# Performance work log

Hardware: AMD Instinct MI355X
Metric: run time of the kernel (lower is better)

Reference implementation:

```python
import jax, jax.numpy as jnp
import numpy as np

DIM = 7
HID = 128
BATCH = 131072
CHOL = DIM * (DIM + 1) // 2  # 28
_TRIL_R, _TRIL_C = np.tril_indices(DIM)
_DIAG = np.arange(DIM)


def _mlp(x, W1, b1, W2, b2, W3, b3):
    h = jnp.tanh(x @ W1 + b1)
    h = jnp.tanh(h @ W2 + b2)
    return h @ W3 + b3


def _build_cholesky(raw):
    # raw: [..., CHOL] -> lower-triangular L [..., DIM, DIM], softplus diagonal for positivity
    L = jnp.zeros(raw.shape[:-1] + (DIM, DIM), raw.dtype)
    L = L.at[..., _TRIL_R, _TRIL_C].set(raw)
    L = L.at[..., _DIAG, _DIAG].set(jax.nn.softplus(L[..., _DIAG, _DIAG]))
    return L


def _spd(raw):
    L = _build_cholesky(raw)
    return L @ jnp.swapaxes(L, -1, -2)  # L L^T, SPD


def setup_inputs() -> dict:
    key = jax.random.key(0)
    ks = jax.random.split(key, 20)
    s = 0.1
    f = jnp.float32
    return {
        "q": jax.random.normal(ks[0], (BATCH, DIM), f),
        "dq": jax.random.normal(ks[1], (BATCH, DIM), f),
        "ddq": jax.random.normal(ks[2], (BATCH, DIM), f),
        "mW1": jax.random.normal(ks[3], (DIM, HID), f) * s,
        "mb1": jax.random.normal(ks[4], (HID,), f) * s,
        "mW2": jax.random.normal(ks[5], (HID, HID), f) * s,
        "mb2": jax.random.normal(ks[6], (HID,), f) * s,
        "mW3": jax.random.normal(ks[7], (HID, CHOL), f) * s,
        "mb3": jax.random.normal(ks[8], (CHOL,), f) * s,
        "dW1": jax.random.normal(ks[9], (2 * DIM, HID), f) * s,
        "db1": jax.random.normal(ks[10], (HID,), f) * s,
        "dW2": jax.random.normal(ks[11], (HID, HID), f) * s,
        "db2": jax.random.normal(ks[12], (HID,), f) * s,
        "dW3": jax.random.normal(ks[13], (HID, CHOL), f) * s,
        "db3": jax.random.normal(ks[14], (CHOL,), f) * s,
        "pW1": jax.random.normal(ks[15], (DIM, HID), f) * s,
        "pb1": jax.random.normal(ks[16], (HID,), f) * s,
        "pw2": jax.random.normal(ks[17], (HID,), f) * s,
    }


def reference(q, dq, ddq, mW1, mb1, mW2, mb2, mW3, mb3,
              dW1, db1, dW2, db2, dW3, db3, pW1, pb1, pw2):
    def M_single(qi):  # qi: [DIM] -> [DIM, DIM]
        return _spd(_mlp(qi, mW1, mb1, mW2, mb2, mW3, mb3))

    # Mass matrix M(q): [B, DIM, DIM]
    Mb = _spd(_mlp(q, mW1, mb1, mW2, mb2, mW3, mb3))

    # Full batched Jacobian dM[i,k]/dq[j] -> J[b,i,k,j], replaces DIM^3 autograd.grad loop
    J = jax.vmap(jax.jacfwd(M_single))(q)  # [B, DIM, DIM, DIM]

    # Coriolis: C[b,i,j] = 0.5 * sum_k (dM_ik/dq_j + dM_ij/dq_k - dM_jk/dq_i) * dq_k
    C = 0.5 * (jnp.einsum('bikj,bk->bij', J, dq)
               + jnp.einsum('bijk,bk->bij', J, dq)
               - jnp.einsum('bjki,bk->bij', J, dq))

    # Damping D(q, dq): [B, DIM, DIM]
    Db = _spd(_mlp(jnp.concatenate([q, dq], axis=1), dW1, db1, dW2, db2, dW3, db3))

    # Convex potential (1-hidden-layer ICNN) and its gradient
    def V_single(qi):
        h = jax.nn.softplus(qi @ pW1 + pb1)
        return h @ jax.nn.softplus(pw2)

    gradV = jax.vmap(jax.grad(V_single))(q)  # [B, DIM]

    tau = (jnp.einsum('bij,bj->bi', Mb, ddq)
           + jnp.einsum('bij,bj->bi', C + Db, dq)
           + gradV)
    return tau
```

## Files before the change

### kernel.cpp

```cpp
#include <hip/hip_runtime.h>

#define DIM 7
#define HID 128
#define CHOL 28

#define GRID_A 512
#define ITER_A 16
#define GRID_B 2048
#define ITER_B 4

#define PHASE_FENCE() __builtin_amdgcn_sched_barrier(0x7F)

typedef float    f32x4  __attribute__((ext_vector_type(4)));
typedef short    bf16x8 __attribute__((ext_vector_type(8)));
typedef unsigned uint4v __attribute__((ext_vector_type(4)));

__device__ __forceinline__ float tanh_f(float x){ float e=__expf(2.f*x); return 1.f - 2.f/(e+1.f); }
__device__ __forceinline__ float sig_f(float x){ return 1.f/(1.f+__expf(-x)); }
__device__ __forceinline__ float sp_f(float x){ return fmaxf(x,0.f) + __logf(1.f+__expf(-fabsf(x))); }

__device__ __forceinline__ unsigned short f2b(float v){
  unsigned u = __float_as_uint(v);
  u += 0x7FFFu + ((u>>16)&1u);
  return (unsigned short)(u>>16);
}
__device__ __forceinline__ bf16x8 as_bf(uint4v u){ union { uint4v a; bf16x8 f; } x; x.a=u; return x.f; }

__global__ void setup_frags(const float* __restrict__ mW2, const float* __restrict__ mW3,
                            const float* __restrict__ dW2, const float* __restrict__ dW3,
                            unsigned* __restrict__ ws){
  int idx = blockIdx.x*256 + threadIdx.x;
  if (idx < 8192) {
    int i2 = idx&3, f = idx>>2, l = f&63, st = f>>6;
    int s = st>>3, t = st&7;
    int k = 32*s + 8*(l>>4) + 2*i2, col = 16*t + (l&15);
    unsigned short lo = f2b(mW2[k*HID+col]), hi = f2b(mW2[(k+1)*HID+col]);
    ws[idx] = (unsigned)lo | ((unsigned)hi<<16);
  } else if (idx < 10240) {
    int j = idx-8192; int i2=j&3, f=j>>2, l=f&63, st=f>>6;
    int s = st>>1, t = st&1;
    int k = 32*s + 8*(l>>4) + 2*i2, col = 16*t + (l&15);
    float v0 = (col<CHOL) ? mW3[k*CHOL+col] : 0.f;
    float v1 = (col<CHOL) ? mW3[(k+1)*CHOL+col] : 0.f;
    ws[idx] = (unsigned)f2b(v0) | ((unsigned)f2b(v1)<<16);
  } else if (idx < 18432) {
    int j = idx-10240; int i2=j&3, f=j>>2, l=f&63, st=f>>6;
    int s = st>>3, t = st&7;
    int k = 32*s + 8*(l>>4) + 2*i2, col = 16*t + (l&15);
    unsigned short lo = f2b(dW2[k*HID+col]), hi = f2b(dW2[(k+1)*HID+col]);
    ws[idx] = (unsigned)lo | ((unsigned)hi<<16);
  } else if (idx < 20480) {
    int j = idx-18432; int i2=j&3, f=j>>2, l=f&63, st=f>>6;
    int s = st>>1, t = st&1;
    int k = 32*s + 8*(l>>4) + 2*i2, col = 16*t + (l&15);
    float v0 = (col<CHOL) ? dW3[k*CHOL+col] : 0.f;
    float v1 = (col<CHOL) ? dW3[(k+1)*CHOL+col] : 0.f;
    ws[idx] = (unsigned)f2b(v0) | ((unsigned)f2b(v1)<<16);
  }
}

__global__ __launch_bounds__(256, 2) void kernA(
    const float* __restrict__ q, const float* __restrict__ dq, const float* __restrict__ ddq,
    const float* __restrict__ mW1, const float* __restrict__ mb1,
    const float* __restrict__ mb2, const float* __restrict__ mb3,
    const float* __restrict__ pW1, const float* __restrict__ pb1, const float* __restrict__ pw2,
    const unsigned* __restrict__ ws, float* __restrict__ out)
{
  __shared__ __align__(16) unsigned short Abuf[4][2][16][HID];
  __shared__ __align__(16) uint4v W3lds[512];
  __shared__ float sbf[4][4][HID+8];
  __shared__ float pW1s[DIM][HID+8];
  __shared__ float rawb[4][4][8][CHOL];
  __shared__ float b2s[HID];
  __shared__ float b3s[CHOL];
  __shared__ float Lbs[4][4][CHOL], dLss[4][4][CHOL], dfs[4][4][CHOL];
  __shared__ float gvp2[4][4][14];
  __shared__ float wbs[4][4][DIM], ubs[4][4][DIM], vss[4][4][DIM];

  const int tid  = threadIdx.x;
  const int wid  = tid>>6;
  const int lane = tid&63;
  const int g4 = lane>>4, c = lane&15;
  const int R = lane&15, r7 = lane&7;

  if (tid < HID) b2s[tid] = mb2[tid];
  if (tid >= HID && tid < HID+CHOL) b3s[tid-HID] = mb3[tid-HID];
  for (int idx = tid; idx < DIM*HID; idx += 256) pW1s[idx>>7][idx&127] = pW1[idx];
  for (int idx = tid; idx < 512; idx += 256) W3lds[idx] = ((const uint4v*)(ws + 8192))[idx];

  float w1v0[DIM], w1v1[DIM], pw1v0[DIM], pw1v1[DIM];
#pragma unroll
  for (int j=0;j<DIM;++j){
    w1v0[j]=mW1[j*HID+lane];  w1v1[j]=mW1[j*HID+lane+64];
    pw1v0[j]=pW1[j*HID+lane]; pw1v1[j]=pW1[j*HID+lane+64];
  }
  const float b1v0=mb1[lane], b1v1=mb1[lane+64];
  const float pbv0=pb1[lane], pbv1=pb1[lane+64];
  const float sp0=sp_f(pw2[lane]), sp1=sp_f(pw2[lane+64]);

  const uint4v* __restrict__ W2f = (const uint4v*)ws;
  uint4v W2r[32];
#pragma unroll
  for (int i=0;i<32;++i) W2r[i] = W2f[i*64 + lane];

  __syncthreads();

  for (int it=0; it<ITER_A; ++it){
    const int ebase = (it*GRID_A + (int)blockIdx.x)*16 + wid*4;

    const int kb0 = lane>>3, ko = lane&7;
#pragma unroll
    for (int e=0;e<4;++e){
      const float* qp = q + (long)(ebase+e)*DIM;
      float qv[DIM];
#pragma unroll
      for (int j=0;j<DIM;++j) qv[j]=qp[j];
      const int mt = e>>1, R0 = 8*(e&1);
      {
        float z1=b1v0, zp=pbv0;
#pragma unroll
        for (int j=0;j<DIM;++j){ z1=fmaf(qv[j],w1v0[j],z1); zp=fmaf(qv[j],pw1v0[j],zp); }
        float h1=tanh_f(z1), g1=1.f-h1*h1;
        Abuf[wid][mt][R0][8*kb0 + ko] = f2b(h1);
#pragma unroll
        for (int j=0;j<DIM;++j)
          Abuf[wid][mt][R0+1+j][8*(kb0^(1+j)) + ko] = f2b(g1*w1v0[j]);
        sbf[wid][e][lane] = sig_f(zp)*sp0;
      }
      {
        float z1=b1v1, zp=pbv1;
#pragma unroll
        for (int j=0;j<DIM;++j){ z1=fmaf(qv[j],w1v1[j],z1); zp=fmaf(qv[j],pw1v1[j],zp); }
        float h1=tanh_f(z1), g1=1.f-h1*h1;
        const int kb1 = kb0+8;
        Abuf[wid][mt][R0][8*kb1 + ko] = f2b(h1);
#pragma unroll
        for (int j=0;j<DIM;++j)
          Abuf[wid][mt][R0+1+j][8*(kb1^(1+j)) + ko] = f2b(g1*w1v1[j]);
        sbf[wid][e][lane+64] = sig_f(zp)*sp1;
      }
    }
    PHASE_FENCE();

    bf16x8 Af0[4], Af1[4];
#pragma unroll
    for (int s=0;s<4;++s){
      const int blk = 8*((4*s+g4)^r7);
      Af0[s] = *(const bf16x8*)&Abuf[wid][0][R][blk];
      Af1[s] = *(const bf16x8*)&Abuf[wid][1][R][blk];
    }
    PHASE_FENCE();

#pragma unroll
    for (int t=0;t<8;++t){
      f32x4 a0 = f32x4{0.f,0.f,0.f,0.f};
      f32x4 a1 = f32x4{0.f,0.f,0.f,0.f};
#pragma unroll
      for (int s=0;s<4;++s){
        bf16x8 B = as_bf(W2r[s*8+t]);
        a0 = __builtin_amdgcn_mfma_f32_16x16x32_bf16(Af0[s],B,a0,0,0,0);
        a1 = __builtin_amdgcn_mfma_f32_16x16x32_bf16(Af1[s],B,a1,0,0,0);
      }
      const int col = 16*t+c;
      const int cb = col>>3, co = col&7;
      {
        const float z2  = a0[0] + b2s[col];
        const float h2o = tanh_f(z2);
        const float h2x = __shfl_xor(h2o, 16);
        const float h2  = (g4&1) ? h2x : h2o;
        const float g2  = 1.f - h2*h2;
#pragma unroll
        for (int reg=0;reg<4;++reg){
          const int Rr = 4*g4+reg;
          const int key = Rr&7;
          float v = g2*a0[reg];
          if (key==0) v = h2;
          Abuf[wid][0][Rr][8*(cb^key) + co] = f2b(v);
        }
      }
      {
        const float z2  = a1[0] + b2s[col];
        const float h2o = tanh_f(z2);
        const float h2x = __shfl_xor(h2o, 16);
        const float h2  = (g4&1) ? h2x : h2o;
        const float g2  = 1.f - h2*h2;
#pragma unroll
        for (int reg=0;reg<4;++reg){
          const int Rr = 4*g4+reg;
          const int key = Rr&7;
          float v = g2*a1[reg];
          if (key==0) v = h2;
          Abuf[wid][1][Rr][8*(cb^key) + co] = f2b(v);
        }
      }
    }
    PHASE_FENCE();

    f32x4 acc3[2][2];
#pragma unroll
    for (int a=0;a<2;++a){ acc3[a][0]=f32x4{0.f,0.f,0.f,0.f}; acc3[a][1]=f32x4{0.f,0.f,0.f,0.f}; }
#pragma unroll
    for (int s=0;s<4;++s){
      const int blk = 8*((4*s+g4)^r7);
      bf16x8 A0 = *(const bf16x8*)&Abuf[wid][0][R][blk];
      bf16x8 A1 = *(const bf16x8*)&Abuf[wid][1][R][blk];
#pragma unroll
      for (int nt=0;nt<2;++nt){
        bf16x8 B = as_bf(W3lds[(s*2+nt)*64 + lane]);
        acc3[0][nt] = __builtin_amdgcn_mfma_f32_16x16x32_bf16(A0,B,acc3[0][nt],0,0,0);
        acc3[1][nt] = __builtin_amdgcn_mfma_f32_16x16x32_bf16(A1,B,acc3[1][nt],0,0,0);
      }
    }

    if (c < 14){
      const int iv = (c<7)? c : c-7;
      const int nb = (c<7)? 0 : 64;
      float gp = 0.f;
#pragma unroll 8
      for (int nn=0; nn<64; ++nn)
        gp = fmaf(pW1s[iv][nb+nn], sbf[wid][g4][nb+nn], gp);
      gvp2[wid][g4][c] = gp;
    }

#pragma unroll
    for (int mt=0;mt<2;++mt){
      const int em = 2*mt + (g4>>1);
      const int rb = (g4&1)*4;
#pragma unroll
      for (int nt=0;nt<2;++nt){
        const int t = 16*nt+c;
        if (t < CHOL){
#pragma unroll
          for (int reg=0;reg<4;++reg) rawb[wid][em][rb+reg][t] = acc3[mt][nt][reg];
        }
      }
    }
    PHASE_FENCE();

    float dqv[DIM];
    {
      const float* dqp = dq + (long)(ebase+g4)*DIM;
#pragma unroll
      for (int j=0;j<DIM;++j) dqv[j]=dqp[j];
    }
#pragma unroll
    for (int h=0;h<2;++h){
      const int t = c + 16*h;
      if (t < CHOL){
        const float e0 = rawb[wid][g4][0][t] + b3s[t];
        const bool dg = (t==0)|(t==2)|(t==5)|(t==9)|(t==14)|(t==20)|(t==27);
        const float Lv = dg ? sp_f(e0) : e0;
        const float df = dg ? sig_f(e0) : 1.f;
        float s_=0.f;
#pragma unroll
        for (int j=0;j<DIM;++j) s_=fmaf(dqv[j], rawb[wid][g4][1+j][t], s_);
        Lbs[wid][g4][t]=Lv; dfs[wid][g4][t]=df; dLss[wid][g4][t]=df*s_;
      }
    }
    PHASE_FENCE();
    if (c < DIM){
      const float* ddqp = ddq + (long)(ebase+g4)*DIM;
      float wv=0.f, uv=0.f, vv=0.f;
#pragma unroll
      for (int r=0;r<DIM;++r){
        if (r>=c){
          const int id=r*(r+1)/2+c;
          const float Lrc = Lbs[wid][g4][id];
          wv=fmaf(Lrc,dqv[r],wv);
          uv=fmaf(Lrc,ddqp[r],uv);
          vv=fmaf(dLss[wid][g4][id],dqv[r],vv);
        }
      }
      wbs[wid][g4][c]=wv; ubs[wid][g4][c]=uv; vss[wid][g4][c]=vv;
    }
    PHASE_FENCE();
    if (c < DIM){
      const int i=c;
      float t12=0.f;
#pragma unroll
      for (int c2=0;c2<DIM;++c2){
        if (c2<=i){
          const int id=i*(i+1)/2+c2;
          t12=fmaf(Lbs[wid][g4][id], ubs[wid][g4][c2]+vss[wid][g4][c2], t12);
          t12=fmaf(dLss[wid][g4][id], wbs[wid][g4][c2], t12);
        }
      }
      const int TRt[CHOL]={0,1,1,2,2,2,3,3,3,3,4,4,4,4,4,5,5,5,5,5,5,6,6,6,6,6,6,6};
      const int TCt[CHOL]={0,0,1,0,1,2,0,1,2,3,0,1,2,3,4,0,1,2,3,4,5,0,1,2,3,4,5,6};
      float t3=0.f;
#pragma unroll
      for (int t=0;t<CHOL;++t)
        t3=fmaf(rawb[wid][g4][1+i][t]*dfs[wid][g4][t], dqv[TRt[t]]*wbs[wid][g4][TCt[t]], t3);
      out[(long)(ebase+g4)*DIM + i] = t12 - t3 + gvp2[wid][g4][i] + gvp2[wid][g4][7+i];
    }
    PHASE_FENCE();
  }
}

__global__ __launch_bounds__(64, 1) void kernB(
    const float* __restrict__ q, const float* __restrict__ dq,
    const float* __restrict__ dW1, const float* __restrict__ db1,
    const float* __restrict__ db2, const float* __restrict__ db3,
    const unsigned* __restrict__ ws, float* __restrict__ out)
{
  __shared__ __align__(16) unsigned short AbufD[16][HID];
  __shared__ float dW1s[2*DIM][HID];
  __shared__ float xsf[112+8], dsf[112+8];
  __shared__ float rawD[16][CHOL];
  __shared__ float LbD[16][CHOL];
  __shared__ float wdb[16][8];
  __shared__ float b2sD[HID];
  __shared__ float b3sD[CHOL];

  const int lane = threadIdx.x;
  const int g4 = lane>>4, c = lane&15;
  const int R = lane&15, rkey = lane&7;
  const int eL = lane>>2, sub = lane&3;

  b2sD[lane] = db2[lane]; b2sD[lane+64] = db2[lane+64];
  if (lane < CHOL) b3sD[lane] = db3[lane];
  for (int idx = lane; idx < 2*DIM*HID; idx += 64) dW1s[idx>>7][idx&127] = dW1[idx];
  const float b1v0 = db1[lane], b1v1 = db1[lane+64];

  const uint4v* __restrict__ W2fD = (const uint4v*)(ws + 10240);
  const uint4v* __restrict__ W3fD = (const uint4v*)(ws + 18432);
  uint4v W2rD[32];
#pragma unroll
  for (int i=0;i<32;++i) W2rD[i] = W2fD[i*64 + lane];
  uint4v W3rD[8];
#pragma unroll
  for (int i=0;i<8;++i)  W3rD[i] = W3fD[i*64 + lane];

  __syncthreads();

  for (int it=0; it<ITER_B; ++it){
    const int ebase = (it*GRID_B + (int)blockIdx.x)*16;

    for (int idx=lane; idx<112; idx+=64){
      xsf[idx] = q[(long)ebase*DIM + idx];
      dsf[idx] = dq[(long)ebase*DIM + idx];
    }
    PHASE_FENCE();

#pragma unroll
    for (int h=0; h<2; ++h){
      const int k = lane + 64*h;
      float z[16];
#pragma unroll
      for (int e=0;e<16;++e) z[e] = h ? b1v1 : b1v0;
#pragma unroll
      for (int j=0;j<DIM;++j){
        const float dj = dW1s[j][k & 127];
#pragma unroll
        for (int e=0;e<16;++e) z[e] = fmaf(xsf[7*e+j], dj, z[e]);
      }
#pragma unroll
      for (int j=0;j<DIM;++j){
        const float dj = dW1s[DIM+j][k & 127];
#pragma unroll
        for (int e=0;e<16;++e) z[e] = fmaf(dsf[7*e+j], dj, z[e]);
      }
      const int kb = k>>3, ko = k&7;
#pragma unroll
      for (int e=0;e<16;++e){
        AbufD[e][8*(kb^(e&7)) + ko] = f2b(tanh_f(z[e]));
      }
    }
    PHASE_FENCE();

    f32x4 acc[8];
#pragma unroll
    for (int b=0;b<8;++b) acc[b] = f32x4{0.f,0.f,0.f,0.f};
#pragma unroll
    for (int s=0;s<4;++s){
      const int blk = 8*((4*s+g4)^rkey);
      bf16x8 A0 = *(const bf16x8*)&AbufD[R][blk];
#pragma unroll
      for (int t=0;t<8;++t)
        acc[t] = __builtin_amdgcn_mfma_f32_16x16x32_bf16(A0, as_bf(W2rD[s*8+t]), acc[t], 0,0,0);
    }
    PHASE_FENCE();

#pragma unroll
    for (int t=0;t<8;++t){
      const int col = 16*t+c;
      const int cb = col>>3, co = col&7;
#pragma unroll
      for (int reg=0;reg<4;++reg){
        const int e = 4*g4+reg;
        const float h2 = tanh_f(acc[t][reg] + b2sD[col]);
        AbufD[e][8*(cb^(e&7)) + co] = f2b(h2);
      }
    }
    PHASE_FENCE();

    f32x4 acc3[2];
    acc3[0]=f32x4{0.f,0.f,0.f,0.f}; acc3[1]=f32x4{0.f,0.f,0.f,0.f};
#pragma unroll
    for (int s=0;s<4;++s){
      const int blk = 8*((4*s+g4)^rkey);
      bf16x8 A0 = *(const bf16x8*)&AbufD[R][blk];
#pragma unroll
      for (int nt=0;nt<2;++nt)
        acc3[nt] = __builtin_amdgcn_mfma_f32_16x16x32_bf16(A0, as_bf(W3rD[s*2+nt]), acc3[nt], 0,0,0);
    }

#pragma unroll
    for (int nt=0;nt<2;++nt){
      const int t = 16*nt+c;
      if (t < CHOL){
#pragma unroll
        for (int reg=0;reg<4;++reg) rawD[4*g4+reg][t] = acc3[nt][reg];
      }
    }
    PHASE_FENCE();

#pragma unroll
    for (int m=0;m<7;++m){
      const int t = 7*sub + m;
      const float e0 = rawD[eL][t] + b3sD[t];
      const bool dg = (t==0)|(t==2)|(t==5)|(t==9)|(t==14)|(t==20)|(t==27);
      LbD[eL][t] = dg ? sp_f(e0) : e0;
    }
    PHASE_FENCE();

    for (int cc = sub; cc < DIM; cc += 4){
      float wv = 0.f;
      for (int r = cc; r < DIM; ++r)
        wv = fmaf(LbD[eL][r*(r+1)/2 + cc], dsf[7*eL + r], wv);
      wdb[eL][cc] = wv;
    }
    PHASE_FENCE();

    for (int i0 = sub; i0 < DIM; i0 += 4){
      float td = 0.f;
      for (int cc = 0; cc <= i0; ++cc)
        td = fmaf(LbD[eL][i0*(i0+1)/2 + cc], wdb[eL][cc], td);
      out[(long)(ebase+eL)*DIM + i0] += td;
    }
    PHASE_FENCE();
  }
}

extern "C" void kernel_launch(void* const* d_in, const int* in_sizes, int n_in,
                              void* d_out, int out_size, void* d_ws, size_t ws_size,
                              hipStream_t stream) {
  const float* q   = (const float*)d_in[0];
  const float* dq  = (const float*)d_in[1];
  const float* ddq = (const float*)d_in[2];
  const float* mW1 = (const float*)d_in[3];
  const float* mb1 = (const float*)d_in[4];
  const float* mW2 = (const float*)d_in[5];
  const float* mb2 = (const float*)d_in[6];
  const float* mW3 = (const float*)d_in[7];
  const float* mb3 = (const float*)d_in[8];
  const float* dW1 = (const float*)d_in[9];
  const float* db1 = (const float*)d_in[10];
  const float* dW2 = (const float*)d_in[11];
  const float* db2 = (const float*)d_in[12];
  const float* dW3 = (const float*)d_in[13];
  const float* db3 = (const float*)d_in[14];
  const float* pW1 = (const float*)d_in[15];
  const float* pb1 = (const float*)d_in[16];
  const float* pw2 = (const float*)d_in[17];
  float* out = (float*)d_out;
  unsigned* wsu = (unsigned*)d_ws;

  hipLaunchKernelGGL(setup_frags, dim3(80), dim3(256), 0, stream, mW2, mW3, dW2, dW3, wsu);
  hipLaunchKernelGGL(kernA, dim3(GRID_A), dim3(256), 0, stream,
                     q, dq, ddq, mW1, mb1, mb2, mb3, pW1, pb1, pw2, (const unsigned*)wsu, out);
  hipLaunchKernelGGL(kernB, dim3(GRID_B), dim3(64), 0, stream,
                     q, dq, dW1, db1, db2, db3, (const unsigned*)wsu, out);
}
```

Baseline: 262.1 us.

## Move W2/W3 weight fragments from registers to LDS and widen blocks to 8 waves

New measurement: 233.8 us. -10.8%, faster.

```diff
diff --git a/kernel.cpp b/kernel.cpp
--- a/kernel.cpp
+++ b/kernel.cpp
@@ -4,9 +4,9 @@
 #define HID 128
 #define CHOL 28
 
-#define GRID_A 512
+#define GRID_A 256
 #define ITER_A 16
-#define GRID_B 2048
+#define GRID_B 256
 #define ITER_B 4
 
 #define PHASE_FENCE() __builtin_amdgcn_sched_barrier(0x7F)
@@ -23,6 +23,9 @@
   unsigned u = __float_as_uint(v);
   u += 0x7FFFu + ((u>>16)&1u);
   return (unsigned short)(u>>16);
+}
+__device__ __forceinline__ float b2f(unsigned short v){
+  return __uint_as_float(((unsigned)v)<<16);
 }
 __device__ __forceinline__ bf16x8 as_bf(uint4v u){ union { uint4v a; bf16x8 f; } x; x.a=u; return x.f; }
 
@@ -59,23 +62,24 @@
   }
 }
 
-__global__ __launch_bounds__(256, 2) void kernA(
+__global__ __launch_bounds__(512, 2) void kernA(
     const float* __restrict__ q, const float* __restrict__ dq, const float* __restrict__ ddq,
     const float* __restrict__ mW1, const float* __restrict__ mb1,
     const float* __restrict__ mb2, const float* __restrict__ mb3,
     const float* __restrict__ pW1, const float* __restrict__ pb1, const float* __restrict__ pw2,
     const unsigned* __restrict__ ws, float* __restrict__ out)
 {
-  __shared__ __align__(16) unsigned short Abuf[4][2][16][HID];
+  __shared__ __align__(16) unsigned short Abuf[8][2][16][HID];
+  __shared__ __align__(16) uint4v W2lds[2048];
   __shared__ __align__(16) uint4v W3lds[512];
-  __shared__ float sbf[4][4][HID+8];
+  __shared__ unsigned short sbf[8][4][HID];
+  __shared__ unsigned short rawb[8][4][8][CHOL];
   __shared__ float pW1s[DIM][HID+8];
-  __shared__ float rawb[4][4][8][CHOL];
   __shared__ float b2s[HID];
   __shared__ float b3s[CHOL];
-  __shared__ float Lbs[4][4][CHOL], dLss[4][4][CHOL], dfs[4][4][CHOL];
-  __shared__ float gvp2[4][4][14];
-  __shared__ float wbs[4][4][DIM], ubs[4][4][DIM], vss[4][4][DIM];
+  __shared__ float Lbs[8][4][CHOL], dLss[8][4][CHOL], dfs[8][4][CHOL];
+  __shared__ float gvp2[8][4][14];
+  __shared__ float wbs[8][4][DIM], ubs[8][4][DIM], vss[8][4][DIM];
 
   const int tid  = threadIdx.x;
   const int wid  = tid>>6;
@@ -85,8 +89,9 @@
 
   if (tid < HID) b2s[tid] = mb2[tid];
   if (tid >= HID && tid < HID+CHOL) b3s[tid-HID] = mb3[tid-HID];
-  for (int idx = tid; idx < DIM*HID; idx += 256) pW1s[idx>>7][idx&127] = pW1[idx];
-  for (int idx = tid; idx < 512; idx += 256) W3lds[idx] = ((const uint4v*)(ws + 8192))[idx];
+  for (int idx = tid; idx < DIM*HID; idx += 512) pW1s[idx>>7][idx&127] = pW1[idx];
+  for (int idx = tid; idx < 2048; idx += 512) W2lds[idx] = ((const uint4v*)ws)[idx];
+  for (int idx = tid; idx < 512;  idx += 512) W3lds[idx] = ((const uint4v*)(ws + 8192))[idx];
 
   float w1v0[DIM], w1v1[DIM], pw1v0[DIM], pw1v1[DIM];
 #pragma unroll
@@ -98,15 +103,10 @@
   const float pbv0=pb1[lane], pbv1=pb1[lane+64];
   const float sp0=sp_f(pw2[lane]), sp1=sp_f(pw2[lane+64]);
 
-  const uint4v* __restrict__ W2f = (const uint4v*)ws;
-  uint4v W2r[32];
-#pragma unroll
-  for (int i=0;i<32;++i) W2r[i] = W2f[i*64 + lane];
-
   __syncthreads();
 
   for (int it=0; it<ITER_A; ++it){
-    const int ebase = (it*GRID_A + (int)blockIdx.x)*16 + wid*4;
+    const int ebase = (it*GRID_A + (int)blockIdx.x)*32 + wid*4;
 
     const int kb0 = lane>>3, ko = lane&7;
 #pragma unroll
@@ -125,7 +125,7 @@
 #pragma unroll
         for (int j=0;j<DIM;++j)
           Abuf[wid][mt][R0+1+j][8*(kb0^(1+j)) + ko] = f2b(g1*w1v0[j]);
-        sbf[wid][e][lane] = sig_f(zp)*sp0;
+        sbf[wid][e][lane] = f2b(sig_f(zp)*sp0);
       }
       {
         float z1=b1v1, zp=pbv1;
@@ -137,7 +137,7 @@
 #pragma unroll
         for (int j=0;j<DIM;++j)
           Abuf[wid][mt][R0+1+j][8*(kb1^(1+j)) + ko] = f2b(g1*w1v1[j]);
-        sbf[wid][e][lane+64] = sig_f(zp)*sp1;
+        sbf[wid][e][lane+64] = f2b(sig_f(zp)*sp1);
       }
     }
     PHASE_FENCE();
@@ -157,7 +157,7 @@
       f32x4 a1 = f32x4{0.f,0.f,0.f,0.f};
 #pragma unroll
       for (int s=0;s<4;++s){
-        bf16x8 B = as_bf(W2r[s*8+t]);
+        bf16x8 B = as_bf(W2lds[(s*8+t)*64 + lane]);
         a0 = __builtin_amdgcn_mfma_f32_16x16x32_bf16(Af0[s],B,a0,0,0,0);
         a1 = __builtin_amdgcn_mfma_f32_16x16x32_bf16(Af1[s],B,a1,0,0,0);
       }
@@ -218,7 +218,7 @@
       float gp = 0.f;
 #pragma unroll 8
       for (int nn=0; nn<64; ++nn)
-        gp = fmaf(pW1s[iv][nb+nn], sbf[wid][g4][nb+nn], gp);
+        gp = fmaf(pW1s[iv][nb+nn], b2f(sbf[wid][g4][nb+nn]), gp);
       gvp2[wid][g4][c] = gp;
     }
 
@@ -231,7 +231,7 @@
         const int t = 16*nt+c;
         if (t < CHOL){
 #pragma unroll
-          for (int reg=0;reg<4;++reg) rawb[wid][em][rb+reg][t] = acc3[mt][nt][reg];
+          for (int reg=0;reg<4;++reg) rawb[wid][em][rb+reg][t] = f2b(acc3[mt][nt][reg]);
         }
       }
     }
@@ -247,13 +247,13 @@
     for (int h=0;h<2;++h){
       const int t = c + 16*h;
       if (t < CHOL){
-        const float e0 = rawb[wid][g4][0][t] + b3s[t];
+        const float e0 = b2f(rawb[wid][g4][0][t]) + b3s[t];
         const bool dg = (t==0)|(t==2)|(t==5)|(t==9)|(t==14)|(t==20)|(t==27);
         const float Lv = dg ? sp_f(e0) : e0;
         const float df = dg ? sig_f(e0) : 1.f;
         float s_=0.f;
 #pragma unroll
-        for (int j=0;j<DIM;++j) s_=fmaf(dqv[j], rawb[wid][g4][1+j][t], s_);
+        for (int j=0;j<DIM;++j) s_=fmaf(dqv[j], b2f(rawb[wid][g4][1+j][t]), s_);
         Lbs[wid][g4][t]=Lv; dfs[wid][g4][t]=df; dLss[wid][g4][t]=df*s_;
       }
     }
@@ -290,55 +290,52 @@
       float t3=0.f;
 #pragma unroll
       for (int t=0;t<CHOL;++t)
-        t3=fmaf(rawb[wid][g4][1+i][t]*dfs[wid][g4][t], dqv[TRt[t]]*wbs[wid][g4][TCt[t]], t3);
+        t3=fmaf(b2f(rawb[wid][g4][1+i][t])*dfs[wid][g4][t], dqv[TRt[t]]*wbs[wid][g4][TCt[t]], t3);
       out[(long)(ebase+g4)*DIM + i] = t12 - t3 + gvp2[wid][g4][i] + gvp2[wid][g4][7+i];
     }
     PHASE_FENCE();
   }
 }
 
-__global__ __launch_bounds__(64, 1) void kernB(
+__global__ __launch_bounds__(512, 2) void kernB(
     const float* __restrict__ q, const float* __restrict__ dq,
     const float* __restrict__ dW1, const float* __restrict__ db1,
     const float* __restrict__ db2, const float* __restrict__ db3,
     const unsigned* __restrict__ ws, float* __restrict__ out)
 {
-  __shared__ __align__(16) unsigned short AbufD[16][HID];
+  __shared__ __align__(16) unsigned short AbufD[8][16][HID];
+  __shared__ __align__(16) uint4v dW2lds[2048];
+  __shared__ __align__(16) uint4v dW3lds[512];
   __shared__ float dW1s[2*DIM][HID];
-  __shared__ float xsf[112+8], dsf[112+8];
-  __shared__ float rawD[16][CHOL];
-  __shared__ float LbD[16][CHOL];
-  __shared__ float wdb[16][8];
+  __shared__ float xsf[8][112+8], dsf[8][112+8];
+  __shared__ float rawD[8][16][CHOL];
+  __shared__ float LbD[8][16][CHOL];
+  __shared__ float wdb[8][16][8];
   __shared__ float b2sD[HID];
   __shared__ float b3sD[CHOL];
 
-  const int lane = threadIdx.x;
+  const int tid  = threadIdx.x;
+  const int wid  = tid>>6;
+  const int lane = tid&63;
   const int g4 = lane>>4, c = lane&15;
   const int R = lane&15, rkey = lane&7;
   const int eL = lane>>2, sub = lane&3;
 
-  b2sD[lane] = db2[lane]; b2sD[lane+64] = db2[lane+64];
-  if (lane < CHOL) b3sD[lane] = db3[lane];
-  for (int idx = lane; idx < 2*DIM*HID; idx += 64) dW1s[idx>>7][idx&127] = dW1[idx];
+  if (tid < HID) b2sD[tid] = db2[tid];
+  if (tid >= HID && tid < HID+CHOL) b3sD[tid-HID] = db3[tid-HID];
+  for (int idx = tid; idx < 2*DIM*HID; idx += 512) dW1s[idx>>7][idx&127] = dW1[idx];
+  for (int idx = tid; idx < 2048; idx += 512) dW2lds[idx] = ((const uint4v*)(ws + 10240))[idx];
+  for (int idx = tid; idx < 512;  idx += 512) dW3lds[idx] = ((const uint4v*)(ws + 18432))[idx];
   const float b1v0 = db1[lane], b1v1 = db1[lane+64];
 
-  const uint4v* __restrict__ W2fD = (const uint4v*)(ws + 10240);
-  const uint4v* __restrict__ W3fD = (const uint4v*)(ws + 18432);
-  uint4v W2rD[32];
-#pragma unroll
-  for (int i=0;i<32;++i) W2rD[i] = W2fD[i*64 + lane];
-  uint4v W3rD[8];
-#pragma unroll
-  for (int i=0;i<8;++i)  W3rD[i] = W3fD[i*64 + lane];
-
   __syncthreads();
 
   for (int it=0; it<ITER_B; ++it){
-    const int ebase = (it*GRID_B + (int)blockIdx.x)*16;
+    const int ebase = (it*GRID_B + (int)blockIdx.x)*128 + wid*16;
 
     for (int idx=lane; idx<112; idx+=64){
-      xsf[idx] = q[(long)ebase*DIM + idx];
-      dsf[idx] = dq[(long)ebase*DIM + idx];
+      xsf[wid][idx] = q[(long)ebase*DIM + idx];
+      dsf[wid][idx] = dq[(long)ebase*DIM + idx];
     }
     PHASE_FENCE();
 
@@ -352,18 +349,18 @@
       for (int j=0;j<DIM;++j){
         const float dj = dW1s[j][k & 127];
 #pragma unroll
-        for (int e=0;e<16;++e) z[e] = fmaf(xsf[7*e+j], dj, z[e]);
+        for (int e=0;e<16;++e) z[e] = fmaf(xsf[wid][7*e+j], dj, z[e]);
       }
 #pragma unroll
       for (int j=0;j<DIM;++j){
         const float dj = dW1s[DIM+j][k & 127];
 #pragma unroll
-        for (int e=0;e<16;++e) z[e] = fmaf(dsf[7*e+j], dj, z[e]);
+        for (int e=0;e<16;++e) z[e] = fmaf(dsf[wid][7*e+j], dj, z[e]);
       }
       const int kb = k>>3, ko = k&7;
 #pragma unroll
       for (int e=0;e<16;++e){
-        AbufD[e][8*(kb^(e&7)) + ko] = f2b(tanh_f(z[e]));
+        AbufD[wid][e][8*(kb^(e&7)) + ko] = f2b(tanh_f(z[e]));
       }
     }
     PHASE_FENCE();
@@ -374,10 +371,10 @@
 #pragma unroll
     for (int s=0;s<4;++s){
       const int blk = 8*((4*s+g4)^rkey);
-      bf16x8 A0 = *(const bf16x8*)&AbufD[R][blk];
+      bf16x8 A0 = *(const bf16x8*)&AbufD[wid][R][blk];
 #pragma unroll
       for (int t=0;t<8;++t)
-        acc[t] = __builtin_amdgcn_mfma_f32_16x16x32_bf16(A0, as_bf(W2rD[s*8+t]), acc[t], 0,0,0);
+        acc[t] = __builtin_amdgcn_mfma_f32_16x16x32_bf16(A0, as_bf(dW2lds[(s*8+t)*64+lane]), acc[t], 0,0,0);
     }
     PHASE_FENCE();
 
@@ -389,7 +386,7 @@
       for (int reg=0;reg<4;++reg){
         const int e = 4*g4+reg;
         const float h2 = tanh_f(acc[t][reg] + b2sD[col]);
-        AbufD[e][8*(cb^(e&7)) + co] = f2b(h2);
+        AbufD[wid][e][8*(cb^(e&7)) + co] = f2b(h2);
       }
     }
     PHASE_FENCE();
@@ -399,10 +396,10 @@
 #pragma unroll
     for (int s=0;s<4;++s){
       const int blk = 8*((4*s+g4)^rkey);
-      bf16x8 A0 = *(const bf16x8*)&AbufD[R][blk];
+      bf16x8 A0 = *(const bf16x8*)&AbufD[wid][R][blk];
 #pragma unroll
       for (int nt=0;nt<2;++nt)
-        acc3[nt] = __builtin_amdgcn_mfma_f32_16x16x32_bf16(A0, as_bf(W3rD[s*2+nt]), acc3[nt], 0,0,0);
+        acc3[nt] = __builtin_amdgcn_mfma_f32_16x16x32_bf16(A0, as_bf(dW3lds[(s*2+nt)*64+lane]), acc3[nt], 0,0,0);
     }
 
 #pragma unroll
@@ -410,7 +407,7 @@
       const int t = 16*nt+c;
       if (t < CHOL){
 #pragma unroll
-        for (int reg=0;reg<4;++reg) rawD[4*g4+reg][t] = acc3[nt][reg];
+        for (int reg=0;reg<4;++reg) rawD[wid][4*g4+reg][t] = acc3[nt][reg];
       }
     }
     PHASE_FENCE();
@@ -418,24 +415,24 @@
 #pragma unroll
     for (int m=0;m<7;++m){
       const int t = 7*sub + m;
-      const float e0 = rawD[eL][t] + b3sD[t];
+      const float e0 = rawD[wid][eL][t] + b3sD[t];
       const bool dg = (t==0)|(t==2)|(t==5)|(t==9)|(t==14)|(t==20)|(t==27);
-      LbD[eL][t] = dg ? sp_f(e0) : e0;
+      LbD[wid][eL][t] = dg ? sp_f(e0) : e0;
     }
     PHASE_FENCE();
 
     for (int cc = sub; cc < DIM; cc += 4){
       float wv = 0.f;
       for (int r = cc; r < DIM; ++r)
-        wv = fmaf(LbD[eL][r*(r+1)/2 + cc], dsf[7*eL + r], wv);
-      wdb[eL][cc] = wv;
+        wv = fmaf(LbD[wid][eL][r*(r+1)/2 + cc], dsf[wid][7*eL + r], wv);
+      wdb[wid][eL][cc] = wv;
     }
     PHASE_FENCE();
 
     for (int i0 = sub; i0 < DIM; i0 += 4){
       float td = 0.f;
       for (int cc = 0; cc <= i0; ++cc)
-        td = fmaf(LbD[eL][i0*(i0+1)/2 + cc], wdb[eL][cc], td);
+        td = fmaf(LbD[wid][eL][i0*(i0+1)/2 + cc], wdb[wid][eL][cc], td);
       out[(long)(ebase+eL)*DIM + i0] += td;
     }
     PHASE_FENCE();
@@ -467,8 +464,8 @@
   unsigned* wsu = (unsigned*)d_ws;
 
   hipLaunchKernelGGL(setup_frags, dim3(80), dim3(256), 0, stream, mW2, mW3, dW2, dW3, wsu);
-  hipLaunchKernelGGL(kernA, dim3(GRID_A), dim3(256), 0, stream,
+  hipLaunchKernelGGL(kernA, dim3(GRID_A), dim3(512), 0, stream,
                      q, dq, ddq, mW1, mb1, mb2, mb3, pW1, pb1, pw2, (const unsigned*)wsu, out);
-  hipLaunchKernelGGL(kernB, dim3(GRID_B), dim3(64), 0, stream,
+  hipLaunchKernelGGL(kernB, dim3(GRID_B), dim3(512), 0, stream,
                      q, dq, dW1, db1, db2, db3, (const unsigned*)wsu, out);
 }
```
